# Performance work log

Measured on AMD Instinct MI355X. Metric: run time of the kernel, lower is better.

The kernel has to match this reference:

```python
import jax, jax.numpy as jnp
from jax import lax
import numpy as np

NUM_CH, LSTM_SIZE, NUM_CLS, SEQ_LEN, NUM_PROPS = 128, 512, 40, 256, 1024

def setup_inputs() -> dict:
    key = jax.random.key(0)
    ks = jax.random.split(key, 16)
    s = 0.05
    H, C = LSTM_SIZE, NUM_CH
    return {
        "data": jax.random.normal(ks[0], (NUM_PROPS, SEQ_LEN, C), jnp.float32),
        "labels": jax.random.randint(ks[1], (NUM_PROPS, 2), 0, NUM_CLS).astype(jnp.int32),
        "proposals": jax.random.uniform(ks[2], (NUM_PROPS, 2), jnp.float32),
        # layer 0 LSTM params (PyTorch gate order i,f,g,o; b = b_ih + b_hh)
        "W_ih_0": jax.random.normal(ks[3], (4 * H, C), jnp.float32) * s,
        "W_hh_0": jax.random.normal(ks[4], (4 * H, H), jnp.float32) * s,
        "b_0": jax.random.normal(ks[5], (4 * H,), jnp.float32) * s,
        # layer 1 LSTM params
        "W_ih_1": jax.random.normal(ks[6], (4 * H, H), jnp.float32) * s,
        "W_hh_1": jax.random.normal(ks[7], (4 * H, H), jnp.float32) * s,
        "b_1": jax.random.normal(ks[8], (4 * H,), jnp.float32) * s,
        # heads
        "W_cls": jax.random.normal(ks[9], (NUM_CLS, H), jnp.float32) * s,
        "b_cls": jnp.zeros((NUM_CLS,), jnp.float32),
        "W_bbox": jax.random.normal(ks[10], (2, H), jnp.float32) * s,
        "b_bbox": jnp.zeros((2,), jnp.float32),
    }

def _lstm_layer(x_tnc, W_ih, W_hh, b):
    # x_tnc: [T, N, C_in]; returns hidden sequence [T, N, H]
    T, N, _ = x_tnc.shape
    H = W_hh.shape[1]
    xg = jnp.einsum('tnc,gc->tng', x_tnc, W_ih) + b  # precompute input projections
    def step(carry, gx):
        h, c = carry
        g = gx + h @ W_hh.T
        i, f, gg, o = jnp.split(g, 4, axis=-1)
        i, f, o = jax.nn.sigmoid(i), jax.nn.sigmoid(f), jax.nn.sigmoid(o)
        c = f * c + i * jnp.tanh(gg)
        h = o * jnp.tanh(c)
        return (h, c), h
    h0 = jnp.zeros((N, H), x_tnc.dtype)
    _, hs = lax.scan(step, (h0, h0), xg)
    return hs

def _forward(data, labels, proposals,
             W_ih_0, W_hh_0, b_0, W_ih_1, W_hh_1, b_1,
             W_cls, b_cls, W_bbox, b_bbox):
    x = jnp.transpose(data, (1, 0, 2))  # [T, N, C]
    x = _lstm_layer(x, W_ih_0, W_hh_0, b_0)
    hs = _lstm_layer(x, W_ih_1, W_hh_1, b_1)
    base_feat = hs[-1]                   # last timestep, [N, H]
    cls_feat = base_feat @ W_cls.T + b_cls
    bbox_feat = base_feat @ W_bbox.T + b_bbox
    # train branch: cross-entropy / loss_div, smooth_l1 * 10
    lbl = labels[:, 0]
    logp = jax.nn.log_softmax(cls_feat, axis=-1)
    cls_loss = -jnp.mean(jnp.take_along_axis(logp, lbl[:, None], axis=1))
    cls_idx = jnp.argmax(cls_feat, axis=1)
    loss_div = 1.0 + jnp.sum((cls_idx == lbl).astype(cls_feat.dtype))
    cls_loss = cls_loss / lax.stop_gradient(loss_div)
    target = proposals / SEQ_LEN
    diff = jnp.abs(bbox_feat - target)
    sl1 = jnp.where(diff < 1.0, 0.5 * diff * diff, diff - 0.5)
    bbox_loss = jnp.mean(sl1) * 10.0
    return jnp.stack([cls_loss, bbox_loss])

def reference(data, labels, proposals,
              W_ih_0, W_hh_0, b_0, W_ih_1, W_hh_1, b_1,
              W_cls, b_cls, W_bbox, b_bbox):
    return _forward(data, labels, proposals,
                    W_ih_0, W_hh_0, b_0, W_ih_1, W_hh_1, b_1,
                    W_cls, b_cls, W_bbox, b_bbox)
```

## Files before the change

### kernel.cpp

```cpp
#include <hip/hip_runtime.h>

typedef unsigned short u16;
typedef __attribute__((ext_vector_type(8))) __bf16 bf16x8;
typedef __attribute__((ext_vector_type(4))) float f32x4;

#define T_SEQ 256
#define N_B   1024
#define C_IN  128
#define H_DIM 512
#define NCLS  40
#define NT0   20
#define NT1   32
#define HSLOT (16*1024*32)

union B8 { bf16x8 v; u16 s[8]; };

__device__ __forceinline__ u16 f32_to_bf16_rne(float x) {
    unsigned u = __float_as_uint(x);
    unsigned rounding = 0x7FFFu + ((u >> 16) & 1u);
    return (u16)((u + rounding) >> 16);
}
__device__ __forceinline__ float bf16_to_f32(u16 h) {
    return __uint_as_float(((unsigned)h) << 16);
}
__device__ __forceinline__ void split2(float x, u16& hi, u16& lo) {
    u16 h = f32_to_bf16_rne(x);
    float hf = bf16_to_f32(h);
    u16 l = f32_to_bf16_rne(x - hf);
    hi = h; lo = l;
}
__device__ __forceinline__ float fast_sigmoid(float x) {
    return 1.0f / (1.0f + __expf(-x));
}
__device__ __forceinline__ float fast_tanh(float x) {
    return 1.0f - 2.0f / (__expf(2.0f * x) + 1.0f);
}

__global__ void k_pack_w(const float* __restrict__ Wih, const float* __restrict__ Whh,
                         int KX, int NT, u16* __restrict__ hi, u16* __restrict__ lo) {
    size_t idx = (size_t)blockIdx.x * 256 + threadIdx.x;
    size_t total = (size_t)16 * NT * 128 * 32;
    if (idx >= total) return;
    int k = (int)(idx & 31);
    int r = (int)((idx >> 5) & 127);
    int rem = (int)(idx >> 12);
    int kt = rem % NT, ct = rem / NT;
    int gate = r & 3, jl = r >> 2;
    int srow = (gate << 9) + (ct << 5) + jl;
    int kg = (kt << 5) + k;
    float v = (kg < KX) ? Wih[(size_t)srow * KX + kg] : Whh[(size_t)srow * H_DIM + (kg - KX)];
    u16 h, l; split2(v, h, l);
    hi[idx] = h; lo[idx] = l;
}

__device__ __forceinline__ void lstm_tile_body(
    int local_blk,
    const float* __restrict__ Xf32,
    const u16* __restrict__ xAhi, const u16* __restrict__ xAlo, int nxt,
    const u16* __restrict__ hAhi, const u16* __restrict__ hAlo,
    const u16* __restrict__ Whi, const u16* __restrict__ Wlo, int NT,
    const float* __restrict__ bias, float* __restrict__ cbuf,
    u16* __restrict__ oHhi, u16* __restrict__ oHlo, float* __restrict__ oF32,
    char* lds, float* biasT)
{
    int ct = ((blockIdx.x & 7) << 1) | ((local_blk >> 6) & 1);
    int rt = (local_blk >> 3) & 7;
    int n0 = rt << 7;

    int tid  = threadIdx.x;
    int w    = tid >> 6;
    int l    = tid & 63;
    int quad = l >> 4;
    int lr   = l & 15;
    int wr   = (w & 1) << 6;
    int wc   = (w >> 1) << 5;

    if (tid < 128)
        biasT[tid] = bias[((tid & 3) << 9) + (ct << 5) + (tid >> 2)];

    const size_t wbase = ((size_t)(ct * NT)) << 12;
    bf16x8 sa_h, sa_l, sb_h, sb_l;

    auto load_stage = [&](int kt) {
        size_t wo = wbase + ((size_t)kt << 12) + ((size_t)tid << 3);
        sb_h = *(const bf16x8*)(Whi + wo);
        sb_l = *(const bf16x8*)(Wlo + wo);
        if (Xf32 != nullptr && kt < nxt) {
            int row = tid >> 2, seg = tid & 3;
            const float* p = Xf32 + (size_t)(n0 + row) * 32768 + (kt << 5) + (seg << 3);
            f32x4 x0 = *(const f32x4*)p;
            f32x4 x1 = *(const f32x4*)(p + 4);
            B8 hh, ll;
            #pragma unroll
            for (int e = 0; e < 4; e++) { u16 a, b; split2(x0[e], a, b); hh.s[e] = a; ll.s[e] = b; }
            #pragma unroll
            for (int e = 0; e < 4; e++) { u16 a, b; split2(x1[e], a, b); hh.s[4 + e] = a; ll.s[4 + e] = b; }
            sa_h = hh.v; sa_l = ll.v;
        } else {
            const u16 *ph, *pl; int kk;
            if (kt < nxt) { ph = xAhi; pl = xAlo; kk = kt; }
            else          { ph = hAhi; pl = hAlo; kk = kt - nxt; }
            size_t ao = (((size_t)kk * 1024 + n0) << 5) + ((size_t)tid << 3);
            sa_h = *(const bf16x8*)(ph + ao);
            sa_l = *(const bf16x8*)(pl + ao);
        }
    };
    auto write_stage = [&](char* buf) {
        *(bf16x8*)(buf + (tid << 4))         = sa_h;
        *(bf16x8*)(buf + 8192 + (tid << 4))  = sa_l;
        *(bf16x8*)(buf + 16384 + (tid << 4)) = sb_h;
        *(bf16x8*)(buf + 24576 + (tid << 4)) = sb_l;
    };

    f32x4 acc[4][2];
    #pragma unroll
    for (int i = 0; i < 4; i++)
        #pragma unroll
        for (int j = 0; j < 2; j++)
            acc[i][j] = (f32x4){0.f, 0.f, 0.f, 0.f};

    load_stage(0);
    write_stage(lds);
    __syncthreads();

    for (int tt = 0; tt < NT; tt++) {
        char* cur = lds + ((tt & 1) << 15);
        if (tt + 1 < NT) load_stage(tt + 1);

        bf16x8 ah[4], al[4], bh[2], bl[2];
        #pragma unroll
        for (int i = 0; i < 4; i++) {
            int ro = (wr + (i << 4) + lr) << 6;
            ah[i] = *(const bf16x8*)(cur + ro + (quad << 4));
            al[i] = *(const bf16x8*)(cur + 8192 + ro + (quad << 4));
        }
        #pragma unroll
        for (int j = 0; j < 2; j++) {
            int ro = (wc + (j << 4) + lr) << 6;
            bh[j] = *(const bf16x8*)(cur + 16384 + ro + (quad << 4));
            bl[j] = *(const bf16x8*)(cur + 24576 + ro + (quad << 4));
        }
        #pragma unroll
        for (int i = 0; i < 4; i++)
            #pragma unroll
            for (int j = 0; j < 2; j++) {
                acc[i][j] = __builtin_amdgcn_mfma_f32_16x16x32_bf16(ah[i], bh[j], acc[i][j], 0, 0, 0);
                acc[i][j] = __builtin_amdgcn_mfma_f32_16x16x32_bf16(al[i], bh[j], acc[i][j], 0, 0, 0);
                acc[i][j] = __builtin_amdgcn_mfma_f32_16x16x32_bf16(ah[i], bl[j], acc[i][j], 0, 0, 0);
            }

        if (tt + 1 < NT) write_stage(lds + (((tt + 1) & 1) << 15));
        __syncthreads();
    }

    float* Gs = (float*)lds;
    #pragma unroll
    for (int i = 0; i < 4; i++)
        #pragma unroll
        for (int j2 = 0; j2 < 2; j2++)
            #pragma unroll
            for (int r = 0; r < 4; r++)
                Gs[(wr + (i << 4) + (quad << 2) + r) * 128 + wc + (j2 << 4) + lr] = acc[i][j2][r];
    __syncthreads();

    int jl = tid & 31;
    int rbase = tid >> 5;
    #pragma unroll
    for (int it = 0; it < 8; it++) {
        int row = rbase + (it << 4);
        f32x4 gv = *(const f32x4*)(Gs + row * 128 + (jl << 2));
        float gi = gv[0] + biasT[(jl << 2) + 0];
        float gf = gv[1] + biasT[(jl << 2) + 1];
        float gg = gv[2] + biasT[(jl << 2) + 2];
        float go = gv[3] + biasT[(jl << 2) + 3];
        float si = fast_sigmoid(gi);
        float sf = fast_sigmoid(gf);
        float so = fast_sigmoid(go);
        int n = n0 + row;
        int cidx = (n << 9) + (ct << 5) + jl;
        float cn = sf * cbuf[cidx] + si * fast_tanh(gg);
        cbuf[cidx] = cn;
        float h = so * fast_tanh(cn);
        u16 hh2, hl2; split2(h, hh2, hl2);
        size_t ho = (((size_t)ct * 1024 + n) << 5) + jl;
        oHhi[ho] = hh2; oHlo[ho] = hl2;
        if (oF32) oF32[cidx] = h;
    }
}

__global__ __launch_bounds__(512) void k_lstm_pair(
    int t, const float* __restrict__ data,
    const u16* __restrict__ W0hi, const u16* __restrict__ W0lo,
    const u16* __restrict__ W1hi, const u16* __restrict__ W1lo,
    const float* __restrict__ b0, const float* __restrict__ b1,
    u16* __restrict__ h0hi, u16* __restrict__ h0lo,
    u16* __restrict__ h1hi, u16* __restrict__ h1lo,
    float* __restrict__ c0, float* __restrict__ c1,
    float* __restrict__ bfeat)
{
    __shared__ __align__(16) char lds[84096];
    __shared__ float biasT[128];
    int local_blk = blockIdx.x & 127;

    if (blockIdx.x < 128) {
        if (t == 0) return;
        int s = t - 1;
        const u16* xh = h0hi + (size_t)(s & 1) * HSLOT;
        const u16* xl = h0lo + (size_t)(s & 1) * HSLOT;
        const u16* hh = h1hi + (size_t)((s - 1) & 1) * HSLOT;
        const u16* hl = h1lo + (size_t)((s - 1) & 1) * HSLOT;
        u16* oh = h1hi + (size_t)(s & 1) * HSLOT;
        u16* ol = h1lo + (size_t)(s & 1) * HSLOT;
        lstm_tile_body(local_blk, nullptr, xh, xl, 16, hh, hl,
                       W1hi, W1lo, NT1, b1, c1, oh, ol,
                       (s == T_SEQ - 1) ? bfeat : nullptr, lds, biasT);
    } else {
        if (t >= T_SEQ) return;
        const u16* hh = h0hi + (size_t)((t - 1) & 1) * HSLOT;
        const u16* hl = h0lo + (size_t)((t - 1) & 1) * HSLOT;
        u16* oh = h0hi + (size_t)(t & 1) * HSLOT;
        u16* ol = h0lo + (size_t)(t & 1) * HSLOT;
        lstm_tile_body(local_blk, data + (size_t)t * C_IN, nullptr, nullptr, 4,
                       hh, hl, W0hi, W0lo, NT0, b0, c0, oh, ol,
                       nullptr, lds, biasT);
    }
}

__global__ __launch_bounds__(64) void k_head(
    const float* __restrict__ hfeat, const float* __restrict__ Wcls, const float* __restrict__ bcls,
    const float* __restrict__ Wbb, const float* __restrict__ bbb,
    const int* __restrict__ labels, const float* __restrict__ props,
    float* __restrict__ accum)
{
    __shared__ float hs[H_DIM];
    __shared__ float logits[NCLS];
    __shared__ float bb[2];
    int n = blockIdx.x, t = threadIdx.x;
    for (int k = t; k < H_DIM; k += 64) hs[k] = hfeat[((size_t)n << 9) + k];
    __syncthreads();
    if (t < NCLS) {
        float s = bcls[t];
        const float* w = Wcls + (size_t)t * H_DIM;
        for (int k = 0; k < H_DIM; k++) s += hs[k] * w[k];
        logits[t] = s;
    } else if (t < NCLS + 2) {
        int j = t - NCLS;
        float s = bbb[j];
        const float* w = Wbb + (size_t)j * H_DIM;
        for (int k = 0; k < H_DIM; k++) s += hs[k] * w[k];
        bb[j] = s;
    }
    __syncthreads();
    if (t == 0) {
        float m = logits[0]; int am = 0;
        for (int j = 1; j < NCLS; j++) if (logits[j] > m) { m = logits[j]; am = j; }
        float se = 0.f;
        for (int j = 0; j < NCLS; j++) se += expf(logits[j] - m);
        int lbl = labels[n * 2];
        float logp = logits[lbl] - m - logf(se);
        atomicAdd(&accum[0], -logp);
        if (am == lbl) atomicAdd(&accum[1], 1.0f);
        float s2 = 0.f;
        for (int j = 0; j < 2; j++) {
            float target = props[n * 2 + j] * (1.0f / 256.0f);
            float d = fabsf(bb[j] - target);
            s2 += (d < 1.f) ? 0.5f * d * d : d - 0.5f;
        }
        atomicAdd(&accum[2], s2);
    }
}

__global__ void k_final(const float* __restrict__ accum, float* __restrict__ out) {
    out[0] = (accum[0] * (1.0f / 1024.0f)) / (1.0f + accum[1]);
    out[1] = accum[2] * (10.0f / 2048.0f);
}

extern "C" void kernel_launch(void* const* d_in, const int* in_sizes, int n_in,
                              void* d_out, int out_size, void* d_ws, size_t ws_size,
                              hipStream_t stream) {
    const float* data  = (const float*)d_in[0];
    const int*   labels= (const int*)d_in[1];
    const float* props = (const float*)d_in[2];
    const float* Wih0  = (const float*)d_in[3];
    const float* Whh0  = (const float*)d_in[4];
    const float* b0    = (const float*)d_in[5];
    const float* Wih1  = (const float*)d_in[6];
    const float* Whh1  = (const float*)d_in[7];
    const float* b1    = (const float*)d_in[8];
    const float* Wcls  = (const float*)d_in[9];
    const float* bcls  = (const float*)d_in[10];
    const float* Wbb   = (const float*)d_in[11];
    const float* bbb   = (const float*)d_in[12];
    float* out = (float*)d_out;

    char* ws = (char*)d_ws;
    size_t off = 0;
    auto alloc = [&](size_t bytes) -> void* {
        void* p = ws + off;
        off = (off + bytes + 255) & ~(size_t)255;
        return p;
    };
    const size_t NH = (size_t)N_B * H_DIM;
    const size_t W0E = (size_t)16 * NT0 * 128 * 32;
    const size_t W1E = (size_t)16 * NT1 * 128 * 32;

    u16* W0hi = (u16*)alloc(W0E * 2);
    u16* W0lo = (u16*)alloc(W0E * 2);
    u16* W1hi = (u16*)alloc(W1E * 2);
    u16* W1lo = (u16*)alloc(W1E * 2);
    u16* h0hi = (u16*)alloc(2 * (size_t)HSLOT * 2);
    u16* h0lo = (u16*)alloc(2 * (size_t)HSLOT * 2);
    u16* h1hi = (u16*)alloc(2 * (size_t)HSLOT * 2);
    u16* h1lo = (u16*)alloc(2 * (size_t)HSLOT * 2);
    float* c0   = (float*)alloc(NH * 4);
    float* c1   = (float*)alloc(NH * 4);
    float* bfeat= (float*)alloc(NH * 4);
    float* accum= (float*)alloc(4 * 4);

    k_pack_w<<<(int)(W0E / 256), 256, 0, stream>>>(Wih0, Whh0, C_IN, NT0, W0hi, W0lo);
    k_pack_w<<<(int)(W1E / 256), 256, 0, stream>>>(Wih1, Whh1, H_DIM, NT1, W1hi, W1lo);

    (void)hipMemsetAsync(h0hi + HSLOT, 0, (size_t)HSLOT * 2, stream);
    (void)hipMemsetAsync(h0lo + HSLOT, 0, (size_t)HSLOT * 2, stream);
    (void)hipMemsetAsync(h1hi + HSLOT, 0, (size_t)HSLOT * 2, stream);
    (void)hipMemsetAsync(h1lo + HSLOT, 0, (size_t)HSLOT * 2, stream);
    (void)hipMemsetAsync(c0, 0, NH * 4, stream);
    (void)hipMemsetAsync(c1, 0, NH * 4, stream);
    (void)hipMemsetAsync(accum, 0, 16, stream);

    for (int t = 0; t <= T_SEQ; t++) {
        k_lstm_pair<<<256, 512, 0, stream>>>(
            t, data, W0hi, W0lo, W1hi, W1lo, b0, b1,
            h0hi, h0lo, h1hi, h1lo, c0, c1, bfeat);
    }

    k_head<<<N_B, 64, 0, stream>>>(bfeat, Wcls, bcls, Wbb, bbb, labels, props, accum);
    k_final<<<1, 1, 0, stream>>>(accum, out);
}
```

Baseline: 8.912 ms.

## Split K across two wave groups with larger per-wave output tiles

The GEMM tile loop now processes two K-tiles per stage. The 8 waves are split into two groups, and each group handles one K-tile with a 64x64 per-wave output tile instead of 64x32. Partial sums from the two groups are written to separate LDS buffers and added in the LSTM epilogue. This halves the number of barrier-separated stages and raises MFMA work per LDS load of A fragments. MFMA issue is also wrapped in s_setprio. The cost is more accumulator registers, LDS use growing to 128KB plus bias, and an extra LDS read and add in the epilogue.

```diff
diff --git a/kernel.cpp b/kernel.cpp
--- a/kernel.cpp
+++ b/kernel.cpp
@@ -72,95 +72,118 @@
     int l    = tid & 63;
     int quad = l >> 4;
     int lr   = l & 15;
+    int grp  = w >> 2;
     int wr   = (w & 1) << 6;
-    int wc   = (w >> 1) << 5;
+    int wc2  = ((w >> 1) & 1) << 6;
 
     if (tid < 128)
         biasT[tid] = bias[((tid & 3) << 9) + (ct << 5) + (tid >> 2)];
 
     const size_t wbase = ((size_t)(ct * NT)) << 12;
-    bf16x8 sa_h, sa_l, sb_h, sb_l;
-
-    auto load_stage = [&](int kt) {
-        size_t wo = wbase + ((size_t)kt << 12) + ((size_t)tid << 3);
-        sb_h = *(const bf16x8*)(Whi + wo);
-        sb_l = *(const bf16x8*)(Wlo + wo);
-        if (Xf32 != nullptr && kt < nxt) {
-            int row = tid >> 2, seg = tid & 3;
-            const float* p = Xf32 + (size_t)(n0 + row) * 32768 + (kt << 5) + (seg << 3);
-            f32x4 x0 = *(const f32x4*)p;
-            f32x4 x1 = *(const f32x4*)(p + 4);
-            B8 hh, ll;
-            #pragma unroll
-            for (int e = 0; e < 4; e++) { u16 a, b; split2(x0[e], a, b); hh.s[e] = a; ll.s[e] = b; }
-            #pragma unroll
-            for (int e = 0; e < 4; e++) { u16 a, b; split2(x1[e], a, b); hh.s[4 + e] = a; ll.s[4 + e] = b; }
-            sa_h = hh.v; sa_l = ll.v;
-        } else {
-            const u16 *ph, *pl; int kk;
-            if (kt < nxt) { ph = xAhi; pl = xAlo; kk = kt; }
-            else          { ph = hAhi; pl = hAlo; kk = kt - nxt; }
-            size_t ao = (((size_t)kk * 1024 + n0) << 5) + ((size_t)tid << 3);
-            sa_h = *(const bf16x8*)(ph + ao);
-            sa_l = *(const bf16x8*)(pl + ao);
+    bf16x8 sa_h[2], sa_l[2], sb_h[2], sb_l[2];
+
+    auto load_stage = [&](int ss) {
+        #pragma unroll
+        for (int g = 0; g < 2; g++) {
+            int kt = (ss << 1) | g;
+            size_t wo = wbase + ((size_t)kt << 12) + ((size_t)tid << 3);
+            sb_h[g] = *(const bf16x8*)(Whi + wo);
+            sb_l[g] = *(const bf16x8*)(Wlo + wo);
+            if (Xf32 != nullptr && kt < nxt) {
+                int row = tid >> 2, seg = tid & 3;
+                const float* p = Xf32 + (size_t)(n0 + row) * 32768 + (kt << 5) + (seg << 3);
+                f32x4 x0 = *(const f32x4*)p;
+                f32x4 x1 = *(const f32x4*)(p + 4);
+                B8 hh, ll;
+                #pragma unroll
+                for (int e = 0; e < 4; e++) { u16 a, b; split2(x0[e], a, b); hh.s[e] = a; ll.s[e] = b; }
+                #pragma unroll
+                for (int e = 0; e < 4; e++) { u16 a, b; split2(x1[e], a, b); hh.s[4 + e] = a; ll.s[4 + e] = b; }
+                sa_h[g] = hh.v; sa_l[g] = ll.v;
+            } else {
+                const u16 *ph, *pl; int kk;
+                if (kt < nxt) { ph = xAhi; pl = xAlo; kk = kt; }
+                else          { ph = hAhi; pl = hAlo; kk = kt - nxt; }
+                size_t ao = (((size_t)kk * 1024 + n0) << 5) + ((size_t)tid << 3);
+                sa_h[g] = *(const bf16x8*)(ph + ao);
+                sa_l[g] = *(const bf16x8*)(pl + ao);
+            }
         }
     };
     auto write_stage = [&](char* buf) {
-        *(bf16x8*)(buf + (tid << 4))         = sa_h;
-        *(bf16x8*)(buf + 8192 + (tid << 4))  = sa_l;
-        *(bf16x8*)(buf + 16384 + (tid << 4)) = sb_h;
-        *(bf16x8*)(buf + 24576 + (tid << 4)) = sb_l;
+        #pragma unroll
+        for (int g = 0; g < 2; g++) {
+            char* p = buf + (g << 13) + (tid << 4);
+            *(bf16x8*)(p)          = sa_h[g];
+            *(bf16x8*)(p + 16384)  = sa_l[g];
+            *(bf16x8*)(p + 32768)  = sb_h[g];
+            *(bf16x8*)(p + 49152)  = sb_l[g];
+        }
     };
 
-    f32x4 acc[4][2];
+    f32x4 acc[4][4];
     #pragma unroll
     for (int i = 0; i < 4; i++)
         #pragma unroll
-        for (int j = 0; j < 2; j++)
+        for (int j = 0; j < 4; j++)
             acc[i][j] = (f32x4){0.f, 0.f, 0.f, 0.f};
 
+    const int NS = NT >> 1;
     load_stage(0);
     write_stage(lds);
     __syncthreads();
 
-    for (int tt = 0; tt < NT; tt++) {
-        char* cur = lds + ((tt & 1) << 15);
-        if (tt + 1 < NT) load_stage(tt + 1);
-
-        bf16x8 ah[4], al[4], bh[2], bl[2];
+    for (int ss = 0; ss < NS; ss++) {
+        char* cur = lds + ((ss & 1) << 16) + (grp << 13);
+        if (ss + 1 < NS) load_stage(ss + 1);
+
+        bf16x8 ah[4], al[4];
         #pragma unroll
         for (int i = 0; i < 4; i++) {
-            int ro = (wr + (i << 4) + lr) << 6;
-            ah[i] = *(const bf16x8*)(cur + ro + (quad << 4));
-            al[i] = *(const bf16x8*)(cur + 8192 + ro + (quad << 4));
-        }
-        #pragma unroll
-        for (int j = 0; j < 2; j++) {
-            int ro = (wc + (j << 4) + lr) << 6;
-            bh[j] = *(const bf16x8*)(cur + 16384 + ro + (quad << 4));
-            bl[j] = *(const bf16x8*)(cur + 24576 + ro + (quad << 4));
-        }
+            int ro = ((wr + (i << 4) + lr) << 6) + (quad << 4);
+            ah[i] = *(const bf16x8*)(cur + ro);
+            al[i] = *(const bf16x8*)(cur + 16384 + ro);
+        }
+        #pragma unroll
+        for (int jp = 0; jp < 2; jp++) {
+            bf16x8 bh[2], bl[2];
+            #pragma unroll
+            for (int u = 0; u < 2; u++) {
+                int j = (jp << 1) | u;
+                int ro = ((wc2 + (j << 4) + lr) << 6) + (quad << 4);
+                bh[u] = *(const bf16x8*)(cur + 32768 + ro);
+                bl[u] = *(const bf16x8*)(cur + 49152 + ro);
+            }
+            __builtin_amdgcn_s_setprio(1);
+            #pragma unroll
+            for (int u = 0; u < 2; u++) {
+                int j = (jp << 1) | u;
+                #pragma unroll
+                for (int i = 0; i < 4; i++) {
+                    acc[i][j] = __builtin_amdgcn_mfma_f32_16x16x32_bf16(ah[i], bh[u], acc[i][j], 0, 0, 0);
+                    acc[i][j] = __builtin_amdgcn_mfma_f32_16x16x32_bf16(al[i], bh[u], acc[i][j], 0, 0, 0);
+                    acc[i][j] = __builtin_amdgcn_mfma_f32_16x16x32_bf16(ah[i], bl[u], acc[i][j], 0, 0, 0);
+                }
+            }
+            __builtin_amdgcn_s_setprio(0);
+        }
+
+        if (ss + 1 < NS) write_stage(lds + (((ss + 1) & 1) << 16));
+        __syncthreads();
+    }
+
+    float* G0 = (float*)lds;
+    float* G1 = (float*)(lds + 65536);
+    {
+        float* myG = grp ? G1 : G0;
         #pragma unroll
         for (int i = 0; i < 4; i++)
             #pragma unroll
-            for (int j = 0; j < 2; j++) {
-                acc[i][j] = __builtin_amdgcn_mfma_f32_16x16x32_bf16(ah[i], bh[j], acc[i][j], 0, 0, 0);
-                acc[i][j] = __builtin_amdgcn_mfma_f32_16x16x32_bf16(al[i], bh[j], acc[i][j], 0, 0, 0);
-                acc[i][j] = __builtin_amdgcn_mfma_f32_16x16x32_bf16(ah[i], bl[j], acc[i][j], 0, 0, 0);
-            }
-
-        if (tt + 1 < NT) write_stage(lds + (((tt + 1) & 1) << 15));
-        __syncthreads();
-    }
-
-    float* Gs = (float*)lds;
-    #pragma unroll
-    for (int i = 0; i < 4; i++)
-        #pragma unroll
-        for (int j2 = 0; j2 < 2; j2++)
-            #pragma unroll
-            for (int r = 0; r < 4; r++)
-                Gs[(wr + (i << 4) + (quad << 2) + r) * 128 + wc + (j2 << 4) + lr] = acc[i][j2][r];
+            for (int j = 0; j < 4; j++)
+                #pragma unroll
+                for (int r = 0; r < 4; r++)
+                    myG[(wr + (i << 4) + (quad << 2) + r) * 128 + wc2 + (j << 4) + lr] = acc[i][j][r];
+    }
     __syncthreads();
 
     int jl = tid & 31;
@@ -168,11 +191,12 @@
     #pragma unroll
     for (int it = 0; it < 8; it++) {
         int row = rbase + (it << 4);
-        f32x4 gv = *(const f32x4*)(Gs + row * 128 + (jl << 2));
-        float gi = gv[0] + biasT[(jl << 2) + 0];
-        float gf = gv[1] + biasT[(jl << 2) + 1];
-        float gg = gv[2] + biasT[(jl << 2) + 2];
-        float go = gv[3] + biasT[(jl << 2) + 3];
+        f32x4 g0 = *(const f32x4*)(G0 + row * 128 + (jl << 2));
+        f32x4 g1 = *(const f32x4*)(G1 + row * 128 + (jl << 2));
+        float gi = g0[0] + g1[0] + biasT[(jl << 2) + 0];
+        float gf = g0[1] + g1[1] + biasT[(jl << 2) + 1];
+        float gg = g0[2] + g1[2] + biasT[(jl << 2) + 2];
+        float go = g0[3] + g1[3] + biasT[(jl << 2) + 3];
         float si = fast_sigmoid(gi);
         float sf = fast_sigmoid(gf);
         float so = fast_sigmoid(go);
@@ -198,7 +222,7 @@
     float* __restrict__ c0, float* __restrict__ c1,
     float* __restrict__ bfeat)
 {
-    __shared__ __align__(16) char lds[84096];
+    __shared__ __align__(16) char lds[131072];
     __shared__ float biasT[128];
     int local_blk = blockIdx.x & 127;
 
```

Result: faster. 7.984 ms (-10.4%).
